# Kernel tuning notes

Measured on AMD Instinct MI355X. Metric: run time of the kernel, lower is better.

The kernel has to match this reference:

```python
import jax, jax.numpy as jnp
import numpy as np

POOLED_H = 7
POOLED_W = 7
SPATIAL_SCALE = 0.25
S = 2  # sampling_ratio (static grid per bin)
ALIGNED_OFFSET = 0.5  # aligned=True


def setup_inputs() -> dict:
    key = jax.random.key(0)
    k1, k2, k3, k4 = jax.random.split(key, 4)
    B, C, H, W = 2, 256, 200, 200
    K = 1000
    x = jax.random.normal(k1, (B, C, H, W), dtype=jnp.float32)
    img_w = W / SPATIAL_SCALE  # 800.0, image-space coords
    img_h = H / SPATIAL_SCALE
    bidx = jax.random.randint(k2, (K,), 0, B).astype(jnp.float32)
    xy1 = jax.random.uniform(k3, (K, 2), dtype=jnp.float32) * jnp.array([img_w * 0.7, img_h * 0.7], jnp.float32)
    wh = jax.random.uniform(k4, (K, 2), dtype=jnp.float32) * jnp.array([img_w * 0.3, img_h * 0.3], jnp.float32) + 1.0
    rois = jnp.concatenate([bidx[:, None], xy1[:, 0:1], xy1[:, 1:2],
                            xy1[:, 0:1] + wh[:, 0:1], xy1[:, 1:2] + wh[:, 1:2]], axis=1)
    return {"x": x, "rois": rois}


def _axis(start, bin_size, pooled, limit):
    """Per-axis sample coords + bilinear corner indices/weights.
    start, bin_size: [K]. Returns low, high [K, pooled*S] int32 and
    w_low, w_high [K, pooled*S] float (validity folded into weights)."""
    p = jnp.arange(pooled, dtype=start.dtype)
    s = (jnp.arange(S, dtype=start.dtype) + 0.5) / S
    coord = start[:, None, None] + (p[None, :, None] + s[None, None, :]) * bin_size[:, None, None]
    coord = coord.reshape(coord.shape[0], pooled * S)  # [K, pooled*S]
    valid = ((coord >= -1.0) & (coord <= limit)).astype(coord.dtype)
    c = jnp.maximum(coord, 0.0)
    low0 = jnp.floor(c).astype(jnp.int32)
    cap = low0 >= limit - 1
    low = jnp.where(cap, limit - 1, low0)
    high = jnp.where(cap, limit - 1, low0 + 1)
    c = jnp.where(cap, low.astype(c.dtype), c)
    l = c - low.astype(c.dtype)
    h = 1.0 - l
    return low, high, h * valid, l * valid


def _roi_align(x, rois):
    B, C, H, W = x.shape
    bidx = rois[:, 0].astype(jnp.int32)
    start_w = rois[:, 1] * SPATIAL_SCALE - ALIGNED_OFFSET
    start_h = rois[:, 2] * SPATIAL_SCALE - ALIGNED_OFFSET
    end_w = rois[:, 3] * SPATIAL_SCALE - ALIGNED_OFFSET
    end_h = rois[:, 4] * SPATIAL_SCALE - ALIGNED_OFFSET
    bin_h = (end_h - start_h) / POOLED_H
    bin_w = (end_w - start_w) / POOLED_W
    yl, yh, wy0, wy1 = _axis(start_h, bin_h, POOLED_H, H)  # [K, PH*S]
    xl, xh, wx0, wx1 = _axis(start_w, bin_w, POOLED_W, W)  # [K, PW*S]
    xt = x.reshape(B, C, H * W).transpose(0, 2, 1)  # [B, HW, C]

    def gather(yi, xi):
        pos = yi[:, :, None] * W + xi[:, None, :]          # [K, NY, NX]
        return xt[bidx[:, None, None], pos, :]             # [K, NY, NX, C]

    out = (wy0[:, :, None, None] * wx0[:, None, :, None] * gather(yl, xl)
         + wy0[:, :, None, None] * wx1[:, None, :, None] * gather(yl, xh)
         + wy1[:, :, None, None] * wx0[:, None, :, None] * gather(yh, xl)
         + wy1[:, :, None, None] * wx1[:, None, :, None] * gather(yh, xh))
    K = rois.shape[0]
    # average over the SxS sample grid inside each bin
    out = out.reshape(K, POOLED_H, S, POOLED_W, S, C).sum(axis=(2, 4)) / float(S * S)
    return out.transpose(0, 3, 1, 2)  # [K, C, PH, PW]


def reference(x, rois):
    return _roi_align(x, rois)
```

## Files before the change

kernel.cpp:

```cpp
#include <hip/hip_runtime.h>
#include <hip/hip_bf16.h>


#define PH 7
#define PW 7
#define SCALE 0.25f
#define C_ 256
#define CH_ 128
#define H_ 200
#define W_ 200
#define HW_ (H_ * W_)

typedef float f32x4 __attribute__((ext_vector_type(4)));

__global__ void __launch_bounds__(512)
transpose_sort_kernel(const float* __restrict__ x, __hip_bfloat16* __restrict__ xt,
                      const float* __restrict__ rois, int K, int mode,
                      int* __restrict__ perm) {
    __shared__ float tile[64][65];
    __shared__ int s[1024];
    int bx = blockIdx.x;
    int tx = threadIdx.x;
    int ty = threadIdx.y;
    int t = ty * 64 + tx;

    if (bx == gridDim.x - 1) {
        if (blockIdx.y != 0 || blockIdx.z != 0) return;
        if (mode == 1) {
            for (int i = t; i < 1024; i += 512) {
                int key = 0x7FFFFFFF;
                if (i < K) {
                    const float* r = rois + (size_t)i * 5;
                    int b = (int)r[0];
                    float yc = (r[2] + r[4]) * (0.5f * SCALE);
                    int yq = min(max((int)yc, 0), 511);
                    key = ((b * 512 + yq) << 12) | i;
                }
                s[i] = key;
            }
            __syncthreads();
            for (int k2 = 2; k2 <= 1024; k2 <<= 1) {
                for (int j = k2 >> 1; j > 0; j >>= 1) {
                    int i = ((t & ~(j - 1)) << 1) | (t & (j - 1));
                    int l = i | j;
                    int a = s[i], b = s[l];
                    bool up = ((i & k2) == 0);
                    if ((a > b) == up) { s[i] = b; s[l] = a; }
                    __syncthreads();
                }
            }
            for (int i = t; i < K; i += 512) perm[i] = s[i] & 0xFFF;
        } else {
            for (int i = t; i < K; i += 512) perm[i] = i;
        }
        return;
    }

    int hw0 = bx * 64;
    int c0  = blockIdx.y * 64;
    int b   = blockIdx.z;
    const float* xb = x + (size_t)b * C_ * HW_;
#pragma unroll
    for (int j = 0; j < 8; ++j) {
        int cl = ty + 8 * j;
        tile[cl][tx] = __builtin_nontemporal_load(&xb[(size_t)(c0 + cl) * HW_ + hw0 + tx]);
    }
    __syncthreads();
    __hip_bfloat16* xtb = xt + (size_t)b * HW_ * C_;
#pragma unroll
    for (int j = 0; j < 8; ++j) {
        int rl = ty + 8 * j;
        xtb[(size_t)(hw0 + rl) * C_ + c0 + tx] = __float2bfloat16(tile[tx][rl]);
    }
}

__device__ __forceinline__ void accum8(float* acc, uint4 v, float w) {
    const unsigned* a = (const unsigned*)&v;
#pragma unroll
    for (int i = 0; i < 4; ++i) {
        acc[2 * i]     = fmaf(w, __uint_as_float(a[i] << 16), acc[2 * i]);
        acc[2 * i + 1] = fmaf(w, __uint_as_float(a[i] & 0xffff0000u), acc[2 * i + 1]);
    }
}

__global__ void __launch_bounds__(512)
roi_main(const __hip_bfloat16* __restrict__ xt, const float* __restrict__ rois,
         const int* __restrict__ perm, float* __restrict__ out, int K, int mode) {
    __shared__ float s_out[CH_ * 49];
    __shared__ int   s_ylo[14], s_yhi[14], s_xlo[14];
    __shared__ float s_wy0[14], s_wy1[14], s_wx0[14], s_wx1[14];
    __shared__ int   s_b;

    int k, chalf;
    if (mode == 1) {
        int xcd  = blockIdx.x & 7;
        int pos  = blockIdx.x >> 3;
        chalf    = xcd >> 2;
        int rank = (xcd & 3) * (K >> 2) + pos;
        k = perm[rank];
    } else {
        int nwg = gridDim.x;
        int q = nwg >> 3, rr = nwg & 7;
        int xcd = blockIdx.x & 7, pos = blockIdx.x >> 3;
        int logical = (xcd < rr ? xcd * (q + 1) : rr * (q + 1) + (xcd - rr) * q) + pos;
        k = perm[logical >> 1];
        chalf = logical & 1;
    }

    int t = threadIdx.x;
    const float* r = rois + (size_t)k * 5;
    if (t == 0) s_b = (int)r[0];
    if (t < 28) {
        bool isy = t < 14;
        int i = isy ? t : t - 14;
        float start = (isy ? r[2] : r[1]) * SCALE - 0.5f;
        float end   = (isy ? r[4] : r[3]) * SCALE - 0.5f;
        float bin = (end - start) * (1.0f / 7.0f);
        int limit = isy ? H_ : W_;
        float pp   = (float)(i >> 1);
        float soff = (i & 1) ? 0.75f : 0.25f;
        float coord = fmaf(pp + soff, bin, start);
        float valid = (coord >= -1.0f && coord <= (float)limit) ? 1.0f : 0.0f;
        float cc = fmaxf(coord, 0.0f);
        int low0 = (int)floorf(cc);
        bool cap = low0 >= limit - 1;
        int lo = cap ? limit - 1 : low0;
        int hi = cap ? limit - 1 : low0 + 1;
        cc = cap ? (float)lo : cc;
        float l = cc - (float)lo;
        float w1 = l * valid, w0 = (1.0f - l) * valid;
        if (isy) {
            s_ylo[i] = lo; s_yhi[i] = hi;
            s_wy0[i] = w0 * 0.25f; s_wy1[i] = w1 * 0.25f;
        } else {
            s_xlo[i] = lo;
            s_wx0[i] = w0; s_wx1[i] = w1;
        }
    }
    __syncthreads();

    int cgi   = t & 15;
    int xc    = (t >> 4) & 1;
    int pslot = t >> 5;

    const __hip_bfloat16* xb = xt + (size_t)s_b * HW_ * C_ + chalf * CH_ + cgi * 8;

    for (int p = pslot; p < 49; p += 16) {
        int ph = p / 7;
        int pw = p - ph * 7;
        int ys0 = 2 * ph, xs0 = 2 * pw;
        int yl0 = s_ylo[ys0],     yh0 = s_yhi[ys0];
        int yl1 = s_ylo[ys0 + 1], yh1 = s_yhi[ys0 + 1];
        int xi0 = s_xlo[xs0] + xc;
        int xi1 = s_xlo[xs0 + 1] + xc;
        float wxa = xc ? s_wx1[xs0]     : s_wx0[xs0];
        float wxb = xc ? s_wx1[xs0 + 1] : s_wx0[xs0 + 1];
        float wA = s_wy0[ys0] * wxa,     wB = s_wy1[ys0] * wxa;
        float wC = s_wy0[ys0] * wxb,     wD = s_wy1[ys0] * wxb;
        float wE = s_wy0[ys0 + 1] * wxa, wF = s_wy1[ys0 + 1] * wxa;
        float wG = s_wy0[ys0 + 1] * wxb, wH = s_wy1[ys0 + 1] * wxb;

        uint4 v0 = *(const uint4*)(xb + ((size_t)(yl0 * W_ + xi0) << 8));
        uint4 v1 = *(const uint4*)(xb + ((size_t)(yh0 * W_ + xi0) << 8));
        uint4 v2 = *(const uint4*)(xb + ((size_t)(yl0 * W_ + xi1) << 8));
        uint4 v3 = *(const uint4*)(xb + ((size_t)(yh0 * W_ + xi1) << 8));
        uint4 v4 = *(const uint4*)(xb + ((size_t)(yl1 * W_ + xi0) << 8));
        uint4 v5 = *(const uint4*)(xb + ((size_t)(yh1 * W_ + xi0) << 8));
        uint4 v6 = *(const uint4*)(xb + ((size_t)(yl1 * W_ + xi1) << 8));
        uint4 v7 = *(const uint4*)(xb + ((size_t)(yh1 * W_ + xi1) << 8));

        float acc[8];
#pragma unroll
        for (int j = 0; j < 8; ++j) acc[j] = 0.0f;
        accum8(acc, v0, wA);
        accum8(acc, v1, wB);
        accum8(acc, v2, wC);
        accum8(acc, v3, wD);
        accum8(acc, v4, wE);
        accum8(acc, v5, wF);
        accum8(acc, v6, wG);
        accum8(acc, v7, wH);

#pragma unroll
        for (int j = 0; j < 8; ++j) {
            float v = acc[j] + __shfl_xor(acc[j], 16, 64);
            if (xc == 0) s_out[(cgi * 8 + j) * 49 + p] = v;
        }
    }
    __syncthreads();

    const f32x4* sv = (const f32x4*)s_out;
    f32x4* ov = (f32x4*)(out + ((size_t)k * C_ + chalf * CH_) * 49);
    for (int i = t; i < (CH_ * 49) / 4; i += 512)
        __builtin_nontemporal_store(sv[i], &ov[i]);
}

__device__ __forceinline__ void axis_sample(float coord, int limit,
                                            int& lo, int& hi,
                                            float& w0, float& w1) {
    float fl = (float)limit;
    float valid = (coord >= -1.0f && coord <= fl) ? 1.0f : 0.0f;
    float c = fmaxf(coord, 0.0f);
    int low0 = (int)floorf(c);
    bool cap = low0 >= limit - 1;
    lo = cap ? limit - 1 : low0;
    hi = cap ? limit - 1 : low0 + 1;
    c = cap ? (float)lo : c;
    float l = c - (float)lo;
    w1 = l * valid;
    w0 = (1.0f - l) * valid;
}

__global__ void __launch_bounds__(256)
roi_align_fallback(const float* __restrict__ x, const float* __restrict__ rois,
                   float* __restrict__ out, int total) {
    int idx = blockIdx.x * blockDim.x + threadIdx.x;
    if (idx >= total) return;
    int pw = idx % PW;
    int ph = (idx / PW) % PH;
    int c  = (idx / (PW * PH)) % C_;
    int k  = idx / (PW * PH * C_);
    const float* r = rois + (size_t)k * 5;
    int b = (int)r[0];
    float start_w = r[1] * SCALE - 0.5f;
    float start_h = r[2] * SCALE - 0.5f;
    float bin_w = (r[3] * SCALE - 0.5f - start_w) / (float)PW;
    float bin_h = (r[4] * SCALE - 0.5f - start_h) / (float)PH;
    const float* xp = x + ((size_t)b * C_ + c) * (size_t)HW_;
    float acc = 0.0f;
#pragma unroll
    for (int sy = 0; sy < 2; ++sy) {
        float yc = start_h + ((float)ph + (sy + 0.5f) * 0.5f) * bin_h;
        int yl, yh; float wy0, wy1;
        axis_sample(yc, H_, yl, yh, wy0, wy1);
        const float* row0 = xp + (size_t)yl * W_;
        const float* row1 = xp + (size_t)yh * W_;
#pragma unroll
        for (int sx = 0; sx < 2; ++sx) {
            float xc2 = start_w + ((float)pw + (sx + 0.5f) * 0.5f) * bin_w;
            int xl, xh; float wx0, wx1;
            axis_sample(xc2, W_, xl, xh, wx0, wx1);
            acc += wy0 * (wx0 * row0[xl] + wx1 * row0[xh])
                 + wy1 * (wx0 * row1[xl] + wx1 * row1[xh]);
        }
    }
    out[idx] = acc * 0.25f;
}

extern "C" void kernel_launch(void* const* d_in, const int* in_sizes, int n_in,
                              void* d_out, int out_size, void* d_ws, size_t ws_size,
                              hipStream_t stream) {
    const float* x    = (const float*)d_in[0];
    const float* rois = (const float*)d_in[1];
    float* out = (float*)d_out;
    int K = in_sizes[1] / 5;
    int B = in_sizes[0] / (C_ * HW_);

    size_t xtbytes = (size_t)B * HW_ * C_ * sizeof(__hip_bfloat16);
    size_t need = xtbytes + 4096 * sizeof(int);
    if (B >= 1 && B <= 8 && ws_size >= need && K <= 4096 && K >= 8) {
        __hip_bfloat16* xt = (__hip_bfloat16*)d_ws;
        int* perm = (int*)((char*)d_ws + xtbytes);
        int mode = (K % 4 == 0 && K <= 1024 && B <= 2) ? 1 : 0;
        dim3 tgrid(HW_ / 64 + 1, C_ / 64, B);
        dim3 tblock(64, 8);
        transpose_sort_kernel<<<tgrid, tblock, 0, stream>>>(x, xt, rois, K, mode, perm);
        roi_main<<<K * 2, 512, 0, stream>>>(xt, rois, perm, out, K, mode);
    } else {
        int total = K * C_ * PH * PW;
        roi_align_fallback<<<(total + 255) / 256, 256, 0, stream>>>(x, rois, out, total);
    }
}
```

Before: 51.72 us.

## Overlap batch-1 transpose with batch-0 ROI pooling in a mixed kernel

Splits the work into three launches: transpose batch 0 plus sorting, then one kernel that interleaves batch-1 transpose tiles with ROI pooling blocks for batch-0 ROIs, and finally ROI pooling for batch-1 ROIs. The aim is to hide the memory-bound transpose of the second image behind the gather-heavy pooling of the first. This adds a third kernel launch and many early-exit blocks, and it drops the XCD-aware block-to-ROI mapping in the mixed kernel.

Result: slower. 66.55 us (+28.7%).

```diff
diff --git a/kernel.cpp b/kernel.cpp
--- a/kernel.cpp
+++ b/kernel.cpp
@@ -10,22 +10,152 @@
 #define H_ 200
 #define W_ 200
 #define HW_ (H_ * W_)
+#define TILES 2500
 
 typedef float f32x4 __attribute__((ext_vector_type(4)));
+
+union SMemU {
+    struct { float tile[64][65]; } a;
+    struct {
+        float s_out[CH_ * 49];
+        int   ylo[14], yhi[14], xlo[14];
+        float wy0[14], wy1[14], wx0[14], wx1[14];
+        int   b;
+    } r;
+};
+
+__device__ __forceinline__ void do_tile(SMemU& sm, const float* __restrict__ x,
+                                        __hip_bfloat16* __restrict__ xt,
+                                        int b, int tt, int t) {
+    int tx = t & 63, ty = t >> 6;
+    int hw0 = (tt % 625) * 64;
+    int c0  = (tt / 625) * 64;
+    const float* xb = x + (size_t)b * C_ * HW_;
+#pragma unroll
+    for (int j = 0; j < 8; ++j) {
+        int cl = ty + 8 * j;
+        sm.a.tile[cl][tx] = __builtin_nontemporal_load(&xb[(size_t)(c0 + cl) * HW_ + hw0 + tx]);
+    }
+    __syncthreads();
+    __hip_bfloat16* xtb = xt + (size_t)b * HW_ * C_;
+#pragma unroll
+    for (int j = 0; j < 8; ++j) {
+        int rl = ty + 8 * j;
+        xtb[(size_t)(hw0 + rl) * C_ + c0 + tx] = __float2bfloat16(sm.a.tile[tx][rl]);
+    }
+}
+
+__device__ __forceinline__ void accum8(float* acc, uint4 v, float w) {
+    const unsigned* a = (const unsigned*)&v;
+#pragma unroll
+    for (int i = 0; i < 4; ++i) {
+        acc[2 * i]     = fmaf(w, __uint_as_float(a[i] << 16), acc[2 * i]);
+        acc[2 * i + 1] = fmaf(w, __uint_as_float(a[i] & 0xffff0000u), acc[2 * i + 1]);
+    }
+}
+
+__device__ __forceinline__ void do_roi(SMemU& sm, const __hip_bfloat16* __restrict__ xt,
+                                       const float* __restrict__ rois,
+                                       float* __restrict__ out,
+                                       int k, int chalf, int t) {
+    const float* r = rois + (size_t)k * 5;
+    if (t == 0) sm.r.b = (int)r[0];
+    if (t < 28) {
+        bool isy = t < 14;
+        int i = isy ? t : t - 14;
+        float start = (isy ? r[2] : r[1]) * SCALE - 0.5f;
+        float end   = (isy ? r[4] : r[3]) * SCALE - 0.5f;
+        float bin = (end - start) * (1.0f / 7.0f);
+        int limit = isy ? H_ : W_;
+        float pp   = (float)(i >> 1);
+        float soff = (i & 1) ? 0.75f : 0.25f;
+        float coord = fmaf(pp + soff, bin, start);
+        float valid = (coord >= -1.0f && coord <= (float)limit) ? 1.0f : 0.0f;
+        float cc = fmaxf(coord, 0.0f);
+        int low0 = (int)floorf(cc);
+        bool cap = low0 >= limit - 1;
+        int lo = cap ? limit - 1 : low0;
+        int hi = cap ? limit - 1 : low0 + 1;
+        cc = cap ? (float)lo : cc;
+        float l = cc - (float)lo;
+        float w1 = l * valid, w0 = (1.0f - l) * valid;
+        if (isy) {
+            sm.r.ylo[i] = lo; sm.r.yhi[i] = hi;
+            sm.r.wy0[i] = w0 * 0.25f; sm.r.wy1[i] = w1 * 0.25f;
+        } else {
+            sm.r.xlo[i] = lo;
+            sm.r.wx0[i] = w0; sm.r.wx1[i] = w1;
+        }
+    }
+    __syncthreads();
+
+    int cgi   = t & 15;
+    int xc    = (t >> 4) & 1;
+    int pslot = t >> 5;
+
+    const __hip_bfloat16* xb = xt + (size_t)sm.r.b * HW_ * C_ + chalf * CH_ + cgi * 8;
+
+    for (int p = pslot; p < 49; p += 16) {
+        int ph = p / 7;
+        int pw = p - ph * 7;
+        int ys0 = 2 * ph, xs0 = 2 * pw;
+        int yl0 = sm.r.ylo[ys0],     yh0 = sm.r.yhi[ys0];
+        int yl1 = sm.r.ylo[ys0 + 1], yh1 = sm.r.yhi[ys0 + 1];
+        int xi0 = sm.r.xlo[xs0] + xc;
+        int xi1 = sm.r.xlo[xs0 + 1] + xc;
+        float wxa = xc ? sm.r.wx1[xs0]     : sm.r.wx0[xs0];
+        float wxb = xc ? sm.r.wx1[xs0 + 1] : sm.r.wx0[xs0 + 1];
+        float wA = sm.r.wy0[ys0] * wxa,     wB = sm.r.wy1[ys0] * wxa;
+        float wC = sm.r.wy0[ys0] * wxb,     wD = sm.r.wy1[ys0] * wxb;
+        float wE = sm.r.wy0[ys0 + 1] * wxa, wF = sm.r.wy1[ys0 + 1] * wxa;
+        float wG = sm.r.wy0[ys0 + 1] * wxb, wH = sm.r.wy1[ys0 + 1] * wxb;
+
+        uint4 v0 = *(const uint4*)(xb + ((size_t)(yl0 * W_ + xi0) << 8));
+        uint4 v1 = *(const uint4*)(xb + ((size_t)(yh0 * W_ + xi0) << 8));
+        uint4 v2 = *(const uint4*)(xb + ((size_t)(yl0 * W_ + xi1) << 8));
+        uint4 v3 = *(const uint4*)(xb + ((size_t)(yh0 * W_ + xi1) << 8));
+        uint4 v4 = *(const uint4*)(xb + ((size_t)(yl1 * W_ + xi0) << 8));
+        uint4 v5 = *(const uint4*)(xb + ((size_t)(yh1 * W_ + xi0) << 8));
+        uint4 v6 = *(const uint4*)(xb + ((size_t)(yl1 * W_ + xi1) << 8));
+        uint4 v7 = *(const uint4*)(xb + ((size_t)(yh1 * W_ + xi1) << 8));
+
+        float acc[8];
+#pragma unroll
+        for (int j = 0; j < 8; ++j) acc[j] = 0.0f;
+        accum8(acc, v0, wA);
+        accum8(acc, v1, wB);
+        accum8(acc, v2, wC);
+        accum8(acc, v3, wD);
+        accum8(acc, v4, wE);
+        accum8(acc, v5, wF);
+        accum8(acc, v6, wG);
+        accum8(acc, v7, wH);
+
+#pragma unroll
+        for (int j = 0; j < 8; ++j) {
+            float v = acc[j] + __shfl_xor(acc[j], 16, 64);
+            if (xc == 0) sm.r.s_out[(cgi * 8 + j) * 49 + p] = v;
+        }
+    }
+    __syncthreads();
+
+    const f32x4* sv = (const f32x4*)sm.r.s_out;
+    f32x4* ov = (f32x4*)(out + ((size_t)k * C_ + chalf * CH_) * 49);
+    for (int i = t; i < (CH_ * 49) / 4; i += 512)
+        __builtin_nontemporal_store(sv[i], &ov[i]);
+}
 
 __global__ void __launch_bounds__(512)
 transpose_sort_kernel(const float* __restrict__ x, __hip_bfloat16* __restrict__ xt,
-                      const float* __restrict__ rois, int K, int mode,
+                      const float* __restrict__ rois, int K, int mode, int B,
                       int* __restrict__ perm) {
-    __shared__ float tile[64][65];
+    __shared__ SMemU sm;
     __shared__ int s[1024];
     int bx = blockIdx.x;
-    int tx = threadIdx.x;
-    int ty = threadIdx.y;
-    int t = ty * 64 + tx;
+    int t = threadIdx.x;
 
     if (bx == gridDim.x - 1) {
-        if (blockIdx.y != 0 || blockIdx.z != 0) return;
+        if (blockIdx.z != 0) return;
         if (mode == 1) {
             for (int i = t; i < 1024; i += 512) {
                 int key = 0x7FFFFFFF;
@@ -55,42 +185,35 @@
         }
         return;
     }
-
-    int hw0 = bx * 64;
-    int c0  = blockIdx.y * 64;
-    int b   = blockIdx.z;
-    const float* xb = x + (size_t)b * C_ * HW_;
-#pragma unroll
-    for (int j = 0; j < 8; ++j) {
-        int cl = ty + 8 * j;
-        tile[cl][tx] = __builtin_nontemporal_load(&xb[(size_t)(c0 + cl) * HW_ + hw0 + tx]);
-    }
-    __syncthreads();
-    __hip_bfloat16* xtb = xt + (size_t)b * HW_ * C_;
-#pragma unroll
-    for (int j = 0; j < 8; ++j) {
-        int rl = ty + 8 * j;
-        xtb[(size_t)(hw0 + rl) * C_ + c0 + tx] = __float2bfloat16(tile[tx][rl]);
-    }
-}
-
-__device__ __forceinline__ void accum8(float* acc, uint4 v, float w) {
-    const unsigned* a = (const unsigned*)&v;
-#pragma unroll
-    for (int i = 0; i < 4; ++i) {
-        acc[2 * i]     = fmaf(w, __uint_as_float(a[i] << 16), acc[2 * i]);
-        acc[2 * i + 1] = fmaf(w, __uint_as_float(a[i] & 0xffff0000u), acc[2 * i + 1]);
-    }
+    do_tile(sm, x, xt, blockIdx.z, bx, t);
+}
+
+__global__ void __launch_bounds__(512)
+mixed_kernel(const float* __restrict__ x, __hip_bfloat16* __restrict__ xt,
+             const float* __restrict__ rois, const int* __restrict__ perm,
+             float* __restrict__ out, int K) {
+    __shared__ SMemU sm;
+    int bid = blockIdx.x;
+    int t = threadIdx.x;
+    if ((bid & 1) == 0) {
+        int tt = bid >> 1;
+        if (tt < TILES) do_tile(sm, x, xt, 1, tt, t);
+        return;
+    }
+    int task = bid >> 1;
+    if (task >= 2 * K) return;
+    int rank  = task >> 1;
+    int chalf = task & 1;
+    int k = perm[rank];
+    if (rois[(size_t)k * 5] >= 0.5f) return;
+    do_roi(sm, xt, rois, out, k, chalf, t);
 }
 
 __global__ void __launch_bounds__(512)
 roi_main(const __hip_bfloat16* __restrict__ xt, const float* __restrict__ rois,
-         const int* __restrict__ perm, float* __restrict__ out, int K, int mode) {
-    __shared__ float s_out[CH_ * 49];
-    __shared__ int   s_ylo[14], s_yhi[14], s_xlo[14];
-    __shared__ float s_wy0[14], s_wy1[14], s_wx0[14], s_wx1[14];
-    __shared__ int   s_b;
-
+         const int* __restrict__ perm, float* __restrict__ out, int K,
+         int mode, int want) {
+    __shared__ SMemU sm;
     int k, chalf;
     if (mode == 1) {
         int xcd  = blockIdx.x & 7;
@@ -106,93 +229,8 @@
         k = perm[logical >> 1];
         chalf = logical & 1;
     }
-
-    int t = threadIdx.x;
-    const float* r = rois + (size_t)k * 5;
-    if (t == 0) s_b = (int)r[0];
-    if (t < 28) {
-        bool isy = t < 14;
-        int i = isy ? t : t - 14;
-        float start = (isy ? r[2] : r[1]) * SCALE - 0.5f;
-        float end   = (isy ? r[4] : r[3]) * SCALE - 0.5f;
-        float bin = (end - start) * (1.0f / 7.0f);
-        int limit = isy ? H_ : W_;
-        float pp   = (float)(i >> 1);
-        float soff = (i & 1) ? 0.75f : 0.25f;
-        float coord = fmaf(pp + soff, bin, start);
-        float valid = (coord >= -1.0f && coord <= (float)limit) ? 1.0f : 0.0f;
-        float cc = fmaxf(coord, 0.0f);
-        int low0 = (int)floorf(cc);
-        bool cap = low0 >= limit - 1;
-        int lo = cap ? limit - 1 : low0;
-        int hi = cap ? limit - 1 : low0 + 1;
-        cc = cap ? (float)lo : cc;
-        float l = cc - (float)lo;
-        float w1 = l * valid, w0 = (1.0f - l) * valid;
-        if (isy) {
-            s_ylo[i] = lo; s_yhi[i] = hi;
-            s_wy0[i] = w0 * 0.25f; s_wy1[i] = w1 * 0.25f;
-        } else {
-            s_xlo[i] = lo;
-            s_wx0[i] = w0; s_wx1[i] = w1;
-        }
-    }
-    __syncthreads();
-
-    int cgi   = t & 15;
-    int xc    = (t >> 4) & 1;
-    int pslot = t >> 5;
-
-    const __hip_bfloat16* xb = xt + (size_t)s_b * HW_ * C_ + chalf * CH_ + cgi * 8;
-
-    for (int p = pslot; p < 49; p += 16) {
-        int ph = p / 7;
-        int pw = p - ph * 7;
-        int ys0 = 2 * ph, xs0 = 2 * pw;
-        int yl0 = s_ylo[ys0],     yh0 = s_yhi[ys0];
-        int yl1 = s_ylo[ys0 + 1], yh1 = s_yhi[ys0 + 1];
-        int xi0 = s_xlo[xs0] + xc;
-        int xi1 = s_xlo[xs0 + 1] + xc;
-        float wxa = xc ? s_wx1[xs0]     : s_wx0[xs0];
-        float wxb = xc ? s_wx1[xs0 + 1] : s_wx0[xs0 + 1];
-        float wA = s_wy0[ys0] * wxa,     wB = s_wy1[ys0] * wxa;
-        float wC = s_wy0[ys0] * wxb,     wD = s_wy1[ys0] * wxb;
-        float wE = s_wy0[ys0 + 1] * wxa, wF = s_wy1[ys0 + 1] * wxa;
-        float wG = s_wy0[ys0 + 1] * wxb, wH = s_wy1[ys0 + 1] * wxb;
-
-        uint4 v0 = *(const uint4*)(xb + ((size_t)(yl0 * W_ + xi0) << 8));
-        uint4 v1 = *(const uint4*)(xb + ((size_t)(yh0 * W_ + xi0) << 8));
-        uint4 v2 = *(const uint4*)(xb + ((size_t)(yl0 * W_ + xi1) << 8));
-        uint4 v3 = *(const uint4*)(xb + ((size_t)(yh0 * W_ + xi1) << 8));
-        uint4 v4 = *(const uint4*)(xb + ((size_t)(yl1 * W_ + xi0) << 8));
-        uint4 v5 = *(const uint4*)(xb + ((size_t)(yh1 * W_ + xi0) << 8));
-        uint4 v6 = *(const uint4*)(xb + ((size_t)(yl1 * W_ + xi1) << 8));
-        uint4 v7 = *(const uint4*)(xb + ((size_t)(yh1 * W_ + xi1) << 8));
-
-        float acc[8];
-#pragma unroll
-        for (int j = 0; j < 8; ++j) acc[j] = 0.0f;
-        accum8(acc, v0, wA);
-        accum8(acc, v1, wB);
-        accum8(acc, v2, wC);
-        accum8(acc, v3, wD);
-        accum8(acc, v4, wE);
-        accum8(acc, v5, wF);
-        accum8(acc, v6, wG);
-        accum8(acc, v7, wH);
-
-#pragma unroll
-        for (int j = 0; j < 8; ++j) {
-            float v = acc[j] + __shfl_xor(acc[j], 16, 64);
-            if (xc == 0) s_out[(cgi * 8 + j) * 49 + p] = v;
-        }
-    }
-    __syncthreads();
-
-    const f32x4* sv = (const f32x4*)s_out;
-    f32x4* ov = (f32x4*)(out + ((size_t)k * C_ + chalf * CH_) * 49);
-    for (int i = t; i < (CH_ * 49) / 4; i += 512)
-        __builtin_nontemporal_store(sv[i], &ov[i]);
+    if (want >= 0 && (int)rois[(size_t)k * 5] != want) return;
+    do_roi(sm, xt, rois, out, k, chalf, threadIdx.x);
 }
 
 __device__ __forceinline__ void axis_sample(float coord, int limit,
@@ -258,14 +296,21 @@
 
     size_t xtbytes = (size_t)B * HW_ * C_ * sizeof(__hip_bfloat16);
     size_t need = xtbytes + 4096 * sizeof(int);
-    if (B >= 1 && B <= 8 && ws_size >= need && K <= 4096 && K >= 8) {
+    bool ok = (B >= 1 && B <= 8 && ws_size >= need && K >= 8 && K <= 1024);
+    if (ok && B == 2 && (K % 4) == 0) {
         __hip_bfloat16* xt = (__hip_bfloat16*)d_ws;
         int* perm = (int*)((char*)d_ws + xtbytes);
-        int mode = (K % 4 == 0 && K <= 1024 && B <= 2) ? 1 : 0;
-        dim3 tgrid(HW_ / 64 + 1, C_ / 64, B);
-        dim3 tblock(64, 8);
-        transpose_sort_kernel<<<tgrid, tblock, 0, stream>>>(x, xt, rois, K, mode, perm);
-        roi_main<<<K * 2, 512, 0, stream>>>(xt, rois, perm, out, K, mode);
+        transpose_sort_kernel<<<dim3(TILES + 1, 1, 1), 512, 0, stream>>>(
+            x, xt, rois, K, 1, B, perm);
+        int g2 = 2 * ((TILES > 2 * K) ? TILES : 2 * K);
+        mixed_kernel<<<g2, 512, 0, stream>>>(x, xt, rois, perm, out, K);
+        roi_main<<<K * 2, 512, 0, stream>>>(xt, rois, perm, out, K, 1, 1);
+    } else if (ok) {
+        __hip_bfloat16* xt = (__hip_bfloat16*)d_ws;
+        int* perm = (int*)((char*)d_ws + xtbytes);
+        transpose_sort_kernel<<<dim3(TILES + 1, 1, B), 512, 0, stream>>>(
+            x, xt, rois, K, 0, B, perm);
+        roi_main<<<K * 2, 512, 0, stream>>>(xt, rois, perm, out, K, 0, -1);
     } else {
         int total = K * C_ * PH * PW;
         roi_align_fallback<<<(total + 255) / 256, 256, 0, stream>>>(x, rois, out, total);
```
